# Performance work log

Measured on AMD Instinct MI355X. Metric: run time of the kernel, lower is better.

## Reference

```python
import jax, jax.numpy as jnp
import numpy as np

RADIUS = 0.1
K = 32  # num_neighbors


def _ball_query(points, centers, radius, k):
    # points: [B,3,N], centers: [B,3,M] -> indices [B,M,K] (int32)
    # PVCNN semantics: first k point indices within radius of each center,
    # unfilled slots padded with the first in-ball index (0 if none in ball).
    N = points.shape[-1]
    p2 = jnp.sum(points * points, axis=1)            # [B,N]
    c2 = jnp.sum(centers * centers, axis=1)          # [B,M]
    cp = jnp.einsum('bdm,bdn->bmn', centers, points)  # [B,M,N]
    dist2 = c2[:, :, None] + p2[:, None, :] - 2.0 * cp
    valid = dist2 < radius * radius                  # [B,M,N]
    # score = point index if in ball else sentinel N; sorting ascending puts
    # the first k in-ball indices (in original point order) up front.
    scores = jnp.where(valid, jnp.arange(N, dtype=jnp.int32), jnp.int32(N))
    idx = jnp.sort(scores, axis=-1)[..., :k]         # [B,M,K]
    first = idx[..., :1]
    first = jnp.where(first == N, 0, first)          # no neighbor -> index 0
    return jnp.where(idx == N, first, idx)


def _group(feat, idx):
    # feat: [B,C,N], idx: [B,M,K] -> [B,C,M,K]
    return jnp.take_along_axis(feat[:, :, None, :], idx[:, None, :, :], axis=3)


def setup_inputs() -> dict:
    key = jax.random.key(0)
    k1, k2, k3 = jax.random.split(key, 3)
    B, N, M, C = 2, 16384, 4096, 32
    points_coords = jax.random.uniform(k1, (B, 3, N), dtype=jnp.float32)
    centers_coords = jax.random.uniform(k2, (B, 3, M), dtype=jnp.float32)
    points_features = jax.random.normal(k3, (B, C, N), dtype=jnp.float32)
    return {
        'points_coords': points_coords,
        'centers_coords': centers_coords,
        'points_features': points_features,
    }


def reference(points_coords, centers_coords, points_features):
    idx = _ball_query(points_coords, centers_coords, RADIUS, K)     # [B,M,K]
    nbr_coords = _group(points_coords, idx)                          # [B,3,M,K]
    nbr_coords = nbr_coords - centers_coords[:, :, :, None]         # relative
    nbr_feats = _group(points_features, idx)                         # [B,C,M,K]
    out = jnp.concatenate([nbr_coords, nbr_feats], axis=1)          # [B,3+C,M,K]
    return jnp.transpose(out, (0, 1, 3, 2))                          # [B,3+C,K,M]
```

## Files before the change

kernel.cpp:

```cpp
#include <hip/hip_runtime.h>

#define B_SZ  2
#define N_PTS 16384
#define M_CTR 4096
#define C_FT  32
#define K_NB  32
#define NCH   35
#define CH_STRIDE (K_NB * M_CTR)
#define CELLS 10
#define NCELL (CELLS * CELLS * CELLS)

__device__ __forceinline__ float fmul(float a, float b) {
    float r; asm("v_mul_f32 %0, %1, %2" : "=v"(r) : "v"(a), "v"(b)); return r;
}
__device__ __forceinline__ float fadd(float a, float b) {
    float r; asm("v_add_f32 %0, %1, %2" : "=v"(r) : "v"(a), "v"(b)); return r;
}
__device__ __forceinline__ float fsub(float a, float b) {
    float r; asm("v_sub_f32 %0, %1, %2" : "=v"(r) : "v"(a), "v"(b)); return r;
}
__device__ __forceinline__ float ffma(float a, float b, float c) {
    float r; asm("v_fma_f32 %0, %1, %2, %3" : "=v"(r) : "v"(a), "v"(b), "v"(c));
    return r;
}

__device__ __forceinline__ bool bq_valid(float x, float y, float z,
                                         float cx, float cy, float cz,
                                         float c2, float r2) {
    const float p2 = fadd(fadd(fmul(x, x), fmul(y, y)), fmul(z, z));
    const float cp = ffma(cz, z, ffma(cy, y, fmul(cx, x)));
    return fsub(fadd(c2, p2), fmul(2.0f, cp)) < r2;
}

__device__ __forceinline__ int cell_of(float x, float y, float z) {
    int ci = (int)(x * 10.0f); ci = ci < 0 ? 0 : (ci > 9 ? 9 : ci);
    int cj = (int)(y * 10.0f); cj = cj < 0 ? 0 : (cj > 9 ? 9 : cj);
    int ck = (int)(z * 10.0f); ck = ck < 0 ? 0 : (ck > 9 ? 9 : ck);
    return (ck * CELLS + cj) * CELLS + ci;
}

__global__ __launch_bounds__(1024) void prep_kernel(
    const float* __restrict__ points,
    const float* __restrict__ feats,
    int* __restrict__ starts,
    int* __restrict__ cursor,
    float* __restrict__ pf)
{
    if (blockIdx.x < B_SZ) {
        const int b = blockIdx.x;
        const int t = threadIdx.x;
        const int lane = t & 63, wid = t >> 6;
        __shared__ int h[NCELL];
        __shared__ int wsum[16];
        for (int c = t; c < NCELL; c += 1024) h[c] = 0;
        __syncthreads();

        const float* __restrict__ px = points + (b * 3 + 0) * N_PTS;
        const float* __restrict__ py = points + (b * 3 + 1) * N_PTS;
        const float* __restrict__ pz = points + (b * 3 + 2) * N_PTS;
#pragma unroll
        for (int i = 0; i < 16; ++i) {
            const int n = t + i * 1024;
            atomicAdd(&h[cell_of(px[n], py[n], pz[n])], 1);
        }
        __syncthreads();

        const int v = (t < NCELL) ? h[t] : 0;
        int incl = v;
        for (int off = 1; off < 64; off <<= 1) {
            const int u = __shfl_up(incl, off);
            if (lane >= off) incl += u;
        }
        if (lane == 63) wsum[wid] = incl;
        __syncthreads();
        if (wid == 0 && lane < 16) {
            const int s = wsum[lane];
            int in2 = s;
            for (int off = 1; off < 16; off <<= 1) {
                const int u = __shfl_up(in2, off);
                if (lane >= off) in2 += u;
            }
            wsum[lane] = in2 - s;
        }
        __syncthreads();
        if (t < NCELL) {
            const int excl = incl - v + wsum[wid];
            starts[b * (NCELL + 1) + t] = excl;
            cursor[b * NCELL + t] = excl;
            if (t == NCELL - 1) starts[b * (NCELL + 1) + NCELL] = excl + v;
        }
    } else {
        __shared__ float tile[64][37];
        const int bid = blockIdx.x - B_SZ;
        const int t  = threadIdx.x;
        const int b  = bid >> 8;
        const int n0 = (bid & 255) * 64;
        for (int i = t; i < NCH * 64; i += 1024) {
            const int r = i >> 6;
            const int c = i & 63;
            float v;
            if (r < 3) v = points[(b * 3 + r) * N_PTS + n0 + c];
            else       v = feats[(b * C_FT + (r - 3)) * N_PTS + n0 + c];
            tile[c][r] = v;
        }
        if (t < 64) tile[t][35] = 0.0f;
        __syncthreads();
        float* __restrict__ dst = pf + ((size_t)b * N_PTS + n0) * 36;
        for (int o = t; o < 64 * 36; o += 1024) {
            const int c = o / 36;
            const int r = o - c * 36;
            dst[o] = tile[c][r];
        }
    }
}

__global__ __launch_bounds__(256) void scatter_kernel(
    const float* __restrict__ points, int* __restrict__ cursor,
    float4* __restrict__ binned) {
    const int t = blockIdx.x * 256 + threadIdx.x;
    const int b = t >> 14, n = t & (N_PTS - 1);
    const float x = points[(b * 3 + 0) * N_PTS + n];
    const float y = points[(b * 3 + 1) * N_PTS + n];
    const float z = points[(b * 3 + 2) * N_PTS + n];
    const int pos = atomicAdd(&cursor[b * NCELL + cell_of(x, y, z)], 1);
    binned[b * N_PTS + pos] = make_float4(x, y, z, __int_as_float(n));
}

__global__ __launch_bounds__(256) void ball_query_kernel(
    const float4* __restrict__ binned,
    const float* __restrict__ centers,
    const int* __restrict__ starts,
    int* __restrict__ idx_out)
{
    const int lane = threadIdx.x & 63;
    const int wid  = threadIdx.x >> 6;
    const int cid  = blockIdx.x * 4 + wid;
    const int b = cid >> 12;
    const int m = cid & (M_CTR - 1);

    const float r2 = (float)(0.1 * 0.1);

    const float cx = centers[(b * 3 + 0) * M_CTR + m];
    const float cy = centers[(b * 3 + 1) * M_CTR + m];
    const float cz = centers[(b * 3 + 2) * M_CTR + m];
    const float c2 = fadd(fadd(fmul(cx, cx), fmul(cy, cy)), fmul(cz, cz));

    __shared__ unsigned bitmap[4][N_PTS / 32];
    unsigned* bm = bitmap[wid];
#pragma unroll
    for (int j = 0; j < 8; ++j) bm[lane * 8 + j] = 0u;

    int ci = (int)(cx * 10.0f); ci = ci < 0 ? 0 : (ci > 9 ? 9 : ci);
    int cj = (int)(cy * 10.0f); cj = cj < 0 ? 0 : (cj > 9 ? 9 : cj);
    int ck = (int)(cz * 10.0f); ck = ck < 0 ? 0 : (ck > 9 ? 9 : ck);
    const int i0 = ci > 0 ? ci - 1 : 0;
    const int i1 = ci < 9 ? ci + 1 : 9;
    const int* st = starts + b * (NCELL + 1);
    const float4* __restrict__ bp = binned + b * N_PTS;

    for (int d = 0; d < 9; ++d) {
        const int jj = cj + (d % 3) - 1;
        const int kk = ck + (d / 3) - 1;
        if (jj < 0 || jj > 9 || kk < 0 || kk > 9) continue;
        const int base = (kk * CELLS + jj) * CELLS;
        const int lo = st[base + i0];
        const int hi = st[base + i1 + 1];
        for (int s0 = lo; s0 < hi; s0 += 64) {
            const int t = s0 + lane;
            if (t < hi) {
                const float4 p = bp[t];
                if (bq_valid(p.x, p.y, p.z, cx, cy, cz, c2, r2)) {
                    const int n = __float_as_int(p.w);
                    atomicOr((int*)&bm[n >> 5], 1 << (n & 31));
                }
            }
        }
    }

    unsigned w[8];
    int cnt = 0;
#pragma unroll
    for (int j = 0; j < 8; ++j) { w[j] = bm[lane * 8 + j]; cnt += __popc(w[j]); }

    int incl = cnt;
    for (int off = 1; off < 64; off <<= 1) {
        const int v = __shfl_up(incl, off);
        if (lane >= off) incl += v;
    }
    const int total = __shfl(incl, 63);
    int slot = incl - cnt;

    int firstbit = 0x7fffffff;
#pragma unroll
    for (int j = 0; j < 8; ++j) {
        if (w[j] && firstbit == 0x7fffffff)
            firstbit = lane * 256 + j * 32 + (__ffs(w[j]) - 1);
    }
    for (int off = 32; off > 0; off >>= 1)
        firstbit = min(firstbit, __shfl_xor(firstbit, off));
    const int first_idx = (total == 0) ? 0 : firstbit;

    int* __restrict__ dst = idx_out + (b * K_NB) * M_CTR + m;
#pragma unroll
    for (int j = 0; j < 8; ++j) {
        unsigned x = w[j];
        while (x && slot < K_NB) {
            const int bit = __ffs(x) - 1;
            dst[slot * M_CTR] = lane * 256 + j * 32 + bit;
            x &= x - 1;
            ++slot;
        }
    }
    if (lane >= total && lane < K_NB) dst[lane * M_CTR] = first_idx;
}

__global__ __launch_bounds__(256) void gather_kernel(
    const float* __restrict__ pf,
    const float* __restrict__ centers,
    const int* __restrict__ idx,
    float* __restrict__ out)
{
    const int t = blockIdx.x * 256 + threadIdx.x;
    const int m = (t & (M_CTR / 2 - 1)) * 2;
    const int k = (t >> 11) & (K_NB - 1);
    const int b = t >> 16;

    const int2 nn = *(const int2*)&idx[(b * K_NB + k) * M_CTR + m];
    const float4* __restrict__ s0 =
        (const float4*)(pf + ((size_t)b * N_PTS + nn.x) * 36);
    const float4* __restrict__ s1 =
        (const float4*)(pf + ((size_t)b * N_PTS + nn.y) * 36);

    float4 f0[9], f1[9];
#pragma unroll
    for (int i = 0; i < 9; ++i) { f0[i] = s0[i]; f1[i] = s1[i]; }

    const float2 cx = *(const float2*)&centers[(b * 3 + 0) * M_CTR + m];
    const float2 cy = *(const float2*)&centers[(b * 3 + 1) * M_CTR + m];
    const float2 cz = *(const float2*)&centers[(b * 3 + 2) * M_CTR + m];

    float v0[36], v1[36];
#pragma unroll
    for (int i = 0; i < 9; ++i) {
        v0[4 * i + 0] = f0[i].x; v0[4 * i + 1] = f0[i].y;
        v0[4 * i + 2] = f0[i].z; v0[4 * i + 3] = f0[i].w;
        v1[4 * i + 0] = f1[i].x; v1[4 * i + 1] = f1[i].y;
        v1[4 * i + 2] = f1[i].z; v1[4 * i + 3] = f1[i].w;
    }
    v0[0] -= cx.x; v0[1] -= cy.x; v0[2] -= cz.x;
    v1[0] -= cx.y; v1[1] -= cy.y; v1[2] -= cz.y;

    float* __restrict__ o = out + ((size_t)b * NCH * K_NB + k) * M_CTR + m;
#pragma unroll
    for (int ch = 0; ch < NCH; ++ch)
        *(float2*)&o[(size_t)ch * CH_STRIDE] = make_float2(v0[ch], v1[ch]);
}

extern "C" void kernel_launch(void* const* d_in, const int* in_sizes, int n_in,
                              void* d_out, int out_size, void* d_ws, size_t ws_size,
                              hipStream_t stream) {
    const float* points  = (const float*)d_in[0];
    const float* centers = (const float*)d_in[1];
    const float* feats   = (const float*)d_in[2];
    float* out = (float*)d_out;

    char* ws = (char*)d_ws;
    int*    idx    = (int*)ws;
    float*  pf     = (float*)(ws + (1u << 20));
    int*    cursor = (int*)(ws + 5716 * 1024);
    int*    starts = (int*)(ws + 5732 * 1024);
    float4* binned = (float4*)(ws + 5764 * 1024);

    prep_kernel<<<B_SZ + B_SZ * (N_PTS / 64), 1024, 0, stream>>>(
        points, feats, starts, cursor, pf);
    scatter_kernel<<<(B_SZ * N_PTS) / 256, 256, 0, stream>>>(
        points, cursor, binned);
    ball_query_kernel<<<(B_SZ * M_CTR) / 4, 256, 0, stream>>>(
        binned, centers, starts, idx);
    gather_kernel<<<(B_SZ * K_NB * M_CTR / 2) / 256, 256, 0, stream>>>(
        pf, centers, idx, out);
}
```

Baseline: 104.5 us.

## Swizzle ball-query bitmap, hoist cell-range loads, use nontemporal output stores

The per-wave LDS bitmap is re-indexed so each lane owns words strided by 64, which should avoid bank conflicts when the bitmap is cleared and read back. Cell indices are made wave-uniform with readfirstlane, and the nine cell start/end ranges are loaded up front so the loads can be batched as scalar loads. The output writes in the gather kernel become nontemporal stores to cut cache pollution from the large streaming output. Word order inside the bitmap changes, so the scan and first-bit logic must still match the new mapping.

```diff
diff --git a/kernel.cpp b/kernel.cpp
--- a/kernel.cpp
+++ b/kernel.cpp
@@ -9,6 +9,8 @@
 #define CH_STRIDE (K_NB * M_CTR)
 #define CELLS 10
 #define NCELL (CELLS * CELLS * CELLS)
+
+typedef float vfloat2 __attribute__((ext_vector_type(2)));
 
 __device__ __forceinline__ float fmul(float a, float b) {
     float r; asm("v_mul_f32 %0, %1, %2" : "=v"(r) : "v"(a), "v"(b)); return r;
@@ -148,30 +150,44 @@
     __shared__ unsigned bitmap[4][N_PTS / 32];
     unsigned* bm = bitmap[wid];
 #pragma unroll
-    for (int j = 0; j < 8; ++j) bm[lane * 8 + j] = 0u;
+    for (int j = 0; j < 8; ++j) bm[j * 64 + lane] = 0u;
 
     int ci = (int)(cx * 10.0f); ci = ci < 0 ? 0 : (ci > 9 ? 9 : ci);
     int cj = (int)(cy * 10.0f); cj = cj < 0 ? 0 : (cj > 9 ? 9 : cj);
     int ck = (int)(cz * 10.0f); ck = ck < 0 ? 0 : (ck > 9 ? 9 : ck);
+    ci = __builtin_amdgcn_readfirstlane(ci);
+    cj = __builtin_amdgcn_readfirstlane(cj);
+    ck = __builtin_amdgcn_readfirstlane(ck);
     const int i0 = ci > 0 ? ci - 1 : 0;
     const int i1 = ci < 9 ? ci + 1 : 9;
     const int* st = starts + b * (NCELL + 1);
     const float4* __restrict__ bp = binned + b * N_PTS;
 
+    int lo_d[9], hi_d[9];
+#pragma unroll
     for (int d = 0; d < 9; ++d) {
         const int jj = cj + (d % 3) - 1;
         const int kk = ck + (d / 3) - 1;
-        if (jj < 0 || jj > 9 || kk < 0 || kk > 9) continue;
-        const int base = (kk * CELLS + jj) * CELLS;
+        const bool ok = (jj >= 0) & (jj <= 9) & (kk >= 0) & (kk <= 9);
+        const int base = ok ? (kk * CELLS + jj) * CELLS : 0;
         const int lo = st[base + i0];
         const int hi = st[base + i1 + 1];
+        lo_d[d] = ok ? lo : 0;
+        hi_d[d] = ok ? hi : 0;
+    }
+
+#pragma unroll
+    for (int d = 0; d < 9; ++d) {
+        const int lo = lo_d[d];
+        const int hi = hi_d[d];
         for (int s0 = lo; s0 < hi; s0 += 64) {
             const int t = s0 + lane;
             if (t < hi) {
                 const float4 p = bp[t];
                 if (bq_valid(p.x, p.y, p.z, cx, cy, cz, c2, r2)) {
                     const int n = __float_as_int(p.w);
-                    atomicOr((int*)&bm[n >> 5], 1 << (n & 31));
+                    atomicOr((int*)&bm[(((n >> 5) & 7) << 6) + (n >> 8)],
+                             1 << (n & 31));
                 }
             }
         }
@@ -180,7 +196,10 @@
     unsigned w[8];
     int cnt = 0;
 #pragma unroll
-    for (int j = 0; j < 8; ++j) { w[j] = bm[lane * 8 + j]; cnt += __popc(w[j]); }
+    for (int j = 0; j < 8; ++j) {
+        w[j] = bm[j * 64 + lane];
+        cnt += __popc(w[j]);
+    }
 
     int incl = cnt;
     for (int off = 1; off < 64; off <<= 1) {
@@ -252,8 +271,10 @@
 
     float* __restrict__ o = out + ((size_t)b * NCH * K_NB + k) * M_CTR + m;
 #pragma unroll
-    for (int ch = 0; ch < NCH; ++ch)
-        *(float2*)&o[(size_t)ch * CH_STRIDE] = make_float2(v0[ch], v1[ch]);
+    for (int ch = 0; ch < NCH; ++ch) {
+        vfloat2 pv; pv.x = v0[ch]; pv.y = v1[ch];
+        __builtin_nontemporal_store(pv, (vfloat2*)&o[(size_t)ch * CH_STRIDE]);
+    }
 }
 
 extern "C" void kernel_launch(void* const* d_in, const int* in_sizes, int n_in,
```

Measured after the change: 104.3 us. Within noise of the previous version (-0.2%).
